# Kernel optimization log

Measured on AMD Instinct MI355X. Metric: run time of the kernel, lower is better.

## Reference

```python
import jax, jax.numpy as jnp
import numpy as np

N_NODES = 50000
N_EDGES = 800000
D_IN = 512
D_HID = 256


def gcn_conv(x, W, b, src, dst, n_nodes):
    """PyG-style GCNConv: self-loops + symmetric normalization.
    x: [N, d_in], W: [d_in, d_out], b: [d_out], src/dst: [E] (already include self-loops? no -> add here)
    """
    loops = jnp.arange(n_nodes, dtype=src.dtype)
    src_f = jnp.concatenate([src, loops])  # [E+N]
    dst_f = jnp.concatenate([dst, loops])
    deg = jax.ops.segment_sum(jnp.ones_like(dst_f, dtype=x.dtype), dst_f,
                              num_segments=n_nodes)  # [N]
    dinv = jnp.where(deg > 0, jax.lax.rsqrt(deg), 0.0)
    norm = dinv[src_f] * dinv[dst_f]  # [E+N]
    h = x @ W  # [N, d_out] -- dense GEMM
    msg = h[src_f] * norm[:, None]  # gather + scale, [E+N, d_out]
    out = jax.ops.segment_sum(msg, dst_f, num_segments=n_nodes)  # scatter-add
    return out + b


def setup_inputs() -> dict:
    key = jax.random.key(0)
    k1, k2, k3, k4, k5 = jax.random.split(key, 5)
    x = jax.random.normal(k1, (N_NODES, D_IN), dtype=jnp.float32)
    edge_index = jax.random.randint(k2, (2, N_EDGES), 0, N_NODES, dtype=jnp.int32)
    # Glorot-ish init for weights
    W1 = jax.random.normal(k3, (D_IN, D_HID), dtype=jnp.float32) / np.sqrt(D_IN)
    W2 = jax.random.normal(k4, (D_HID, D_HID), dtype=jnp.float32) / np.sqrt(D_HID)
    b1 = jnp.zeros((D_HID,), dtype=jnp.float32)
    b2 = jnp.zeros((D_HID,), dtype=jnp.float32)
    return {"x": x, "edge_index": edge_index, "W1": W1, "b1": b1, "W2": W2, "b2": b2}


def reference(x, edge_index, W1, b1, W2, b2):
    n_nodes = x.shape[0]
    src, dst = edge_index[0], edge_index[1]
    h = jax.nn.relu(gcn_conv(x, W1, b1, src, dst, n_nodes))
    h = gcn_conv(h, W2, b2, src, dst, n_nodes)
    # edge-level gather-dot scoring
    score = jnp.einsum('ed,ed->e', h[src], h[dst])  # [E]
    prob_edge = jax.nn.sigmoid(score)
    return prob_edge
```

## Files before the change

kernel.cpp:

```cpp
#include <hip/hip_runtime.h>
#include <stdint.h>

#define D_IN 512
#define D_HID 256

typedef __attribute__((ext_vector_type(8))) short bf16x8;
typedef __attribute__((ext_vector_type(8))) unsigned short u16x8;
typedef __attribute__((ext_vector_type(4))) float f32x4;

__device__ __forceinline__ float b2f(unsigned short u) {
    union { float f; uint32_t i; } x; x.i = ((uint32_t)u) << 16; return x.f;
}
__device__ __forceinline__ unsigned short f2b(float f) {
    union { float f; uint32_t i; } x; x.f = f;
    uint32_t i = x.i;
    uint32_t r = (i + 0x7FFFu + ((i >> 16) & 1u)) >> 16;
    return (unsigned short)r;
}

__device__ __forceinline__ void async_copy16(const unsigned short* g, unsigned short* lds) {
    __builtin_amdgcn_global_load_lds((const __attribute__((address_space(1))) unsigned int*)g,
                                     (__attribute__((address_space(3))) unsigned int*)lds,
                                     16, 0, 0);
}

__global__ __launch_bounds__(256) void detect_dtype_kernel(const ushort4* __restrict__ raw,
        int n4, int* __restrict__ flag, int* __restrict__ counts, int N, int dblocks) {
    int b = blockIdx.x;
    if (b >= dblocks) {
        int i = (b - dblocks) * 256 + threadIdx.x;
        if (i < N) counts[i] = 0;
        return;
    }
    int i = b * 256 + threadIdx.x;
    int hit = 0;
    if (i < n4) {
        ushort4 u = raw[i];
        hit = ((((u.x >> 7) & 0xFF) == 0xFF) || (((u.y >> 7) & 0xFF) == 0xFF) ||
               (((u.z >> 7) & 0xFF) == 0xFF) || (((u.w >> 7) & 0xFF) == 0xFF)) ? 1 : 0;
    }
    unsigned long long bl = __ballot(hit);
    if ((threadIdx.x & 63) == 0 && bl != 0ULL) atomicOr(flag, 1);
}

__device__ __forceinline__ void wpack_body(const void* __restrict__ W,
        unsigned short* __restrict__ Wp, int K, bool f32, int t) {
    int total = (K >> 6) * 2 * 16 * 64;
    if (t >= total) return;
    int lane = t & 63;
    int c = (t >> 6) & 15;
    int h = (t >> 10) & 1;
    int kk = t >> 11;
    int n = c * 16 + (lane & 15);
    int k0 = kk * 64 + h * 32 + (lane >> 4) * 8;
    u16x8 o;
#pragma unroll
    for (int j = 0; j < 8; ++j) {
        float v = f32 ? ((const float*)W)[(size_t)(k0 + j) * 256 + n]
                      : b2f(((const unsigned short*)W)[(size_t)(k0 + j) * 256 + n]);
        o[j] = f2b(v);
    }
    *(u16x8*)(Wp + (size_t)t * 8) = o;
}

__global__ __launch_bounds__(256) void pre_fused_kernel(const int* __restrict__ dst,
        int* __restrict__ counts, int* __restrict__ within, int E,
        const void* __restrict__ W1, unsigned short* __restrict__ Wp1,
        const void* __restrict__ W2, unsigned short* __restrict__ Wp2,
        const int* __restrict__ flag, int histBlocks, int wp1Blocks) {
    int b = blockIdx.x;
    if (b < histBlocks) {
        int halfE = (E + 1) >> 1;
        int e = b * 256 + threadIdx.x;
        if (e < halfE) {
            int d1 = dst[e];
            int e2 = e + halfE;
            if (e2 < E) {
                int d2 = dst[e2];
                within[e]  = atomicAdd(&counts[d1], 1);
                within[e2] = atomicAdd(&counts[d2], 1);
            } else {
                within[e] = atomicAdd(&counts[d1], 1);
            }
        }
        return;
    }
    b -= histBlocks;
    bool f32 = (*flag != 0);
    if (b < wp1Blocks) {
        wpack_body(W1, Wp1, D_IN, f32, b * 256 + threadIdx.x);
    } else {
        wpack_body(W2, Wp2, D_HID, f32, (b - wp1Blocks) * 256 + threadIdx.x);
    }
}

__global__ __launch_bounds__(256) void partial_sum_kernel(const int* __restrict__ counts,
        int* __restrict__ partial, int n) {
    __shared__ int sh[4];
    int b = blockIdx.x;
    int lane = threadIdx.x & 63, wv = threadIdx.x >> 6;
    int s = 0;
    for (int j = threadIdx.x; j < 1024; j += 256) {
        int i = b * 1024 + j;
        s += (i < n) ? counts[i] : 0;
    }
#pragma unroll
    for (int off = 32; off > 0; off >>= 1) s += __shfl_down(s, off, 64);
    if (lane == 0) sh[wv] = s;
    __syncthreads();
    if (threadIdx.x == 0) partial[b] = sh[0] + sh[1] + sh[2] + sh[3];
}

__global__ void scan_partials_kernel(int* __restrict__ partial, int nb,
                                     int* __restrict__ indptr, int N) {
    int lane = threadIdx.x & 63;
    int orig = (lane < nb) ? partial[lane] : 0;
    int v = orig;
#pragma unroll
    for (int off = 1; off < 64; off <<= 1) {
        int u = __shfl(v, lane - off, 64);
        if (lane >= off) v += u;
    }
    int tot = __shfl(v, nb - 1, 64);
    if (lane < nb) partial[lane] = v - orig;
    if (lane == 0) indptr[N] = tot;
}

__global__ __launch_bounds__(1024) void scan_chunk_kernel(const int* __restrict__ counts,
        const int* __restrict__ partial, int* __restrict__ indptr,
        float* __restrict__ dinv, int n) {
    __shared__ int sh[1024];
    int b = blockIdx.x;
    int i = b * 1024 + threadIdx.x;
    int v = (i < n) ? counts[i] : 0;
    sh[threadIdx.x] = v;
    __syncthreads();
    for (int off = 1; off < 1024; off <<= 1) {
        int t = (threadIdx.x >= off) ? sh[threadIdx.x - off] : 0;
        __syncthreads();
        sh[threadIdx.x] += t;
        __syncthreads();
    }
    if (i < n) {
        int e = partial[b] + sh[threadIdx.x] - v;
        indptr[i] = e;
        dinv[i] = rsqrtf((float)(v + 1));
    }
}

template<int K, bool MF32, bool FUSE>
__global__ __launch_bounds__(256) void gemm_bf16(const void* __restrict__ Ain,
        const unsigned short* __restrict__ Wp, unsigned short* __restrict__ C, int M,
        const int* __restrict__ flag,
        const int* __restrict__ eidx, const int* __restrict__ within,
        int* __restrict__ csr_src, int* __restrict__ csr_dst, int* __restrict__ pos_of,
        const int* __restrict__ indptr, int E, int sblocks) {
    __shared__ unsigned short As[(K == 256) ? 4 : 2][64 * 64];
    constexpr int NK = K / 64;
    int bid = blockIdx.x;
    int gblocks = (M + 63) >> 6;
    if (FUSE) {
        if (bid >= gblocks) {
            int tb = bid - gblocks;
            if (tb < sblocks) {
                int e = tb * 256 + (int)threadIdx.x;
                if (e < E) {
                    int d = eidx[(size_t)E + e];
                    int pos = indptr[d] + within[e];
                    csr_src[pos] = eidx[e];
                    pos_of[e] = pos;
                }
            } else {
                int v = (tb - sblocks) * 256 + (int)threadIdx.x;
                if (v < M) {
                    int b0 = indptr[v], e0 = indptr[v + 1];
                    for (int p = b0; p < e0; ++p) csr_dst[p] = v;
                }
            }
            return;
        }
    }
    int t = threadIdx.x;
    int lane = t & 63, wv = t >> 6;
    int n0 = lane & 15, grp = lane >> 4;
    int row0 = bid * 64;

    int srow = wv * 16 + (lane >> 3);
    int segp = lane & 7;

    f32x4 acc[4][4];
#pragma unroll
    for (int rt = 0; rt < 4; ++rt)
#pragma unroll
        for (int ct = 0; ct < 4; ++ct) acc[rt][ct] = (f32x4){0.f, 0.f, 0.f, 0.f};

    auto compute_tile = [&](int kk, const unsigned short* Abuf) {
        bf16x8 bw[4][2];
#pragma unroll
        for (int ct = 0; ct < 4; ++ct)
#pragma unroll
            for (int h = 0; h < 2; ++h)
                bw[ct][h] = *(const bf16x8*)(Wp +
                    ((size_t)(((kk * 2 + h) * 16) + (wv * 4 + ct)) * 64 + lane) * 8);
#pragma unroll
        for (int rt = 0; rt < 4; ++rt) {
            int r = rt * 16 + n0;
#pragma unroll
            for (int h = 0; h < 2; ++h) {
                int sp = (h * 4 + grp + r) & 7;
                bf16x8 a = *(const bf16x8*)(Abuf + r * 64 + sp * 8);
#pragma unroll
                for (int ct = 0; ct < 4; ++ct)
                    acc[rt][ct] = __builtin_amdgcn_mfma_f32_16x16x32_bf16(a, bw[ct][h],
                                                                          acc[rt][ct], 0, 0, 0);
            }
        }
    };

    bool f32src = MF32 && (*flag != 0);
    if (f32src) {
        const float* A = (const float*)Ain;
        auto stage_f32 = [&](int buf, const float4* pr) {
#pragma unroll
            for (int j = 0; j < 2; ++j) {
                u16x8 o;
#pragma unroll
                for (int q = 0; q < 4; ++q) {
                    o[q]     = f2b(pr[j * 2 + 0][q]);
                    o[q + 4] = f2b(pr[j * 2 + 1][q]);
                }
                *(u16x8*)(&As[buf][0] + wv * 1024 + j * 512 + lane * 8) = o;
            }
        };
        auto load_f32 = [&](int kof, float4* pr) {
#pragma unroll
            for (int j = 0; j < 2; ++j) {
                int row = srow + j * 8;
                int s = (segp - row) & 7;
                const float* g = A + (size_t)min(row0 + row, M - 1) * K + kof + s * 8;
                pr[j * 2 + 0] = *(const float4*)(g);
                pr[j * 2 + 1] = *(const float4*)(g + 4);
            }
        };
        float4 pr[4];
        load_f32(0, pr);
        stage_f32(0, pr);
        for (int kk = 0; kk < NK; ++kk) {
            int cur = kk & 1;
            if (kk + 1 < NK) load_f32((kk + 1) * 64, pr);
            asm volatile("s_waitcnt lgkmcnt(0)" ::: "memory");
            __builtin_amdgcn_s_barrier();
            compute_tile(kk, &As[cur][0]);
            if (kk + 1 < NK) stage_f32(cur ^ 1, pr);
        }
    } else if constexpr (K == 256) {
        const unsigned short* A = (const unsigned short*)Ain;
#pragma unroll
        for (int kk = 0; kk < 4; ++kk) {
#pragma unroll
            for (int j = 0; j < 2; ++j) {
                int row = srow + j * 8;
                int s = (segp - row) & 7;
                const unsigned short* g = A + (size_t)min(row0 + row, M - 1) * K
                                           + kk * 64 + s * 8;
                async_copy16(g, &As[kk][0] + wv * 1024 + j * 512);
            }
        }
        asm volatile("s_waitcnt vmcnt(0)" ::: "memory");
        __builtin_amdgcn_s_barrier();
#pragma unroll
        for (int kk = 0; kk < 4; ++kk) compute_tile(kk, &As[kk][0]);
    } else {
        const unsigned short* A = (const unsigned short*)Ain;
#pragma unroll
        for (int j = 0; j < 2; ++j) {
            int row = srow + j * 8;
            int s = (segp - row) & 7;
            const unsigned short* g = A + (size_t)min(row0 + row, M - 1) * K + s * 8;
            async_copy16(g, &As[0][0] + wv * 1024 + j * 512);
        }
        asm volatile("s_waitcnt vmcnt(0)" ::: "memory");
        __builtin_amdgcn_s_barrier();
        for (int kk = 0; kk < NK; ++kk) {
            int cur = kk & 1;
            if (kk + 1 < NK) {
                int kof = (kk + 1) * 64;
#pragma unroll
                for (int j = 0; j < 2; ++j) {
                    int row = srow + j * 8;
                    int s = (segp - row) & 7;
                    const unsigned short* g = A + (size_t)min(row0 + row, M - 1) * K + kof + s * 8;
                    async_copy16(g, &As[cur ^ 1][0] + wv * 1024 + j * 512);
                }
            }
            compute_tile(kk, &As[cur][0]);
            asm volatile("s_waitcnt vmcnt(0)" ::: "memory");
            __builtin_amdgcn_s_barrier();
        }
    }
#pragma unroll
    for (int rt = 0; rt < 4; ++rt) {
#pragma unroll
        for (int ct = 0; ct < 4; ++ct) {
#pragma unroll
            for (int reg = 0; reg < 4; ++reg) {
                int row = row0 + rt * 16 + grp * 4 + reg;
                if (row < M)
                    C[(size_t)row * 256 + (wv * 4 + ct) * 16 + n0] = f2b(acc[rt][ct][reg]);
            }
        }
    }
}

__global__ __launch_bounds__(256) void aggregate_kernel(const unsigned short* __restrict__ h,
        const int* __restrict__ indptr, const int* __restrict__ csr_src,
        const float* __restrict__ dinv, const void* __restrict__ bias,
        unsigned short* __restrict__ out, int n, int do_relu, const int* __restrict__ flag) {
    int wave = threadIdx.x >> 6;
    int lane = threadIdx.x & 63;
    int half = lane >> 5;
    int hl = lane & 31;
    int v = blockIdx.x * 4 + wave;
    if (v >= n) return;
    int beg = indptr[v];
    int end = indptr[v + 1];
    float dv = dinv[v];

    float acc[8];
    if (half == 0) {
        u16x8 hv = *(const u16x8*)(h + (size_t)v * 256 + hl * 8);
#pragma unroll
        for (int i = 0; i < 8; ++i) acc[i] = dv * b2f(hv[i]);
    } else {
#pragma unroll
        for (int i = 0; i < 8; ++i) acc[i] = 0.f;
    }

    float wA = 0.f, wB = 0.f, wC = 0.f;
    u16x8 rA = (u16x8)0, rB = (u16x8)0, rC = (u16x8)0;
    auto ld = [&](int idx, float& w, u16x8& r) {
        if (idx < end) {
            int s = csr_src[idx];
            w = dinv[s];
            r = *(const u16x8*)(h + (size_t)s * 256 + hl * 8);
        } else {
            w = 0.f;
        }
    };
    int e = beg + half;
    ld(e, wA, rA);
    ld(e + 2, wB, rB);
    ld(e + 4, wC, rC);
    while (e + 4 < end) {
#pragma unroll
        for (int i = 0; i < 8; ++i) acc[i] += wA * b2f(rA[i]);
        ld(e + 6, wA, rA);
#pragma unroll
        for (int i = 0; i < 8; ++i) acc[i] += wB * b2f(rB[i]);
        ld(e + 8, wB, rB);
#pragma unroll
        for (int i = 0; i < 8; ++i) acc[i] += wC * b2f(rC[i]);
        ld(e + 10, wC, rC);
        e += 6;
    }
#pragma unroll
    for (int i = 0; i < 8; ++i)
        acc[i] += wA * b2f(rA[i]) + wB * b2f(rB[i]) + wC * b2f(rC[i]);

#pragma unroll
    for (int i = 0; i < 8; ++i) acc[i] += __shfl_xor(acc[i], 32, 64);

    if (half == 0) {
        float bb[8];
        if (*flag != 0) {
            const float* bp = (const float*)bias + hl * 8;
#pragma unroll
            for (int i = 0; i < 8; ++i) bb[i] = bp[i];
        } else {
            const unsigned short* bp = (const unsigned short*)bias + hl * 8;
#pragma unroll
            for (int i = 0; i < 8; ++i) bb[i] = b2f(bp[i]);
        }
        u16x8 ov;
#pragma unroll
        for (int i = 0; i < 8; ++i) {
            float o = dv * acc[i] + bb[i];
            if (do_relu) o = fmaxf(o, 0.f);
            ov[i] = f2b(o);
        }
        *(u16x8*)(out + (size_t)v * 256 + hl * 8) = ov;
    }
}

__global__ __launch_bounds__(256) void edge_score_mfma(const unsigned short* __restrict__ h,
        const int* __restrict__ csr_src, const int* __restrict__ csr_dst,
        float* __restrict__ tmp, int E) {
    int lane = threadIdx.x & 63;
    int wv = threadIdx.x >> 6;
    int base = (blockIdx.x * 4 + wv) * 16;
    if (base >= E) return;
    int m = lane & 15, grp = lane >> 4;
    int e = base + m;
    int ec = min(e, E - 1);
    int s = csr_src[ec], d = csr_dst[ec];
    const unsigned short* hs = h + (size_t)s * 256 + grp * 8;
    const unsigned short* hd = h + (size_t)d * 256 + grp * 8;
    f32x4 acc = {0.f, 0.f, 0.f, 0.f};
#pragma unroll
    for (int kk = 0; kk < 8; ++kk) {
        bf16x8 a = *(const bf16x8*)(hs + kk * 32);
        bf16x8 b = *(const bf16x8*)(hd + kk * 32);
        acc = __builtin_amdgcn_mfma_f32_16x16x32_bf16(a, b, acc, 0, 0, 0);
    }
    int reg = m - grp * 4;
    if (reg >= 0 && reg < 4 && e < E) {
        float p = (reg == 0) ? acc[0] : (reg == 1) ? acc[1] : (reg == 2) ? acc[2] : acc[3];
        tmp[e] = 1.f / (1.f + __expf(-p));
    }
}

__global__ __launch_bounds__(256) void permute_out_kernel(const float* __restrict__ tmp,
        const int* __restrict__ pos_of, void* __restrict__ out, int E,
        const int* __restrict__ flag) {
    int e = blockIdx.x * blockDim.x + threadIdx.x;
    if (e >= E) return;
    float p = tmp[pos_of[e]];
    if (*flag != 0)
        ((float*)out)[e] = p;
    else
        ((unsigned short*)out)[e] = f2b(p);
}

extern "C" void kernel_launch(void* const* d_in, const int* in_sizes, int n_in,
                              void* d_out, int out_size, void* d_ws, size_t ws_size,
                              hipStream_t stream) {
    const void* x  = d_in[0];
    const int* edge_index = (const int*)d_in[1];
    const void* W1 = d_in[2];
    const void* b1 = d_in[3];
    const void* W2 = d_in[4];
    const void* b2 = d_in[5];

    const int N = in_sizes[0] / D_IN;
    const int E = in_sizes[1] / 2;
    const int* dst = edge_index + E;

    char* ws = (char*)d_ws;
    size_t off = 0;
    auto alloc = [&](size_t bytes) {
        char* p = ws + off;
        off = (off + bytes + 255) & ~(size_t)255;
        return p;
    };
    int* flag     = (int*)alloc(256);
    float* dinv   = (float*)alloc((size_t)N * 4);
    int* counts   = (int*)alloc((size_t)N * 4);
    int* indptr   = (int*)alloc((size_t)(N + 1) * 4);
    int* partial  = (int*)alloc(64 * 4);
    int* within   = (int*)alloc((size_t)E * 4);
    int* csr_src  = (int*)alloc((size_t)E * 4);
    int* csr_dst  = (int*)alloc((size_t)E * 4);
    int* pos_of   = (int*)alloc((size_t)E * 4);
    float* ptmp   = (float*)alloc((size_t)E * 4);
    unsigned short* Wp1 = (unsigned short*)alloc((size_t)D_IN * 256 * 2);
    unsigned short* Wp2 = (unsigned short*)alloc((size_t)D_HID * 256 * 2);
    unsigned short* hA  = (unsigned short*)alloc((size_t)N * 256 * 2);
    unsigned short* hB  = (unsigned short*)alloc((size_t)N * 256 * 2);

    const int nb = (N + 1023) / 1024;
    const int halfE = (E + 1) / 2;
    const int histBlocks = (halfE + 255) / 256;
    const int sblocks = (E + 255) / 256;
    const int fblocks = (N + 255) / 256;
    const int wp1Blocks = (D_IN * 32) / 256;
    const int wp2Blocks = (D_HID * 32) / 256;
    const int ggrid = (N + 63) / 64;
    const int dblocks = 64;

    hipMemsetAsync(flag, 0, 4, stream);
    detect_dtype_kernel<<<dblocks + fblocks, 256, 0, stream>>>(
        (const ushort4*)x, 16384, flag, counts, N, dblocks);
    pre_fused_kernel<<<histBlocks + wp1Blocks + wp2Blocks, 256, 0, stream>>>(
        dst, counts, within, E, W1, Wp1, W2, Wp2, flag, histBlocks, wp1Blocks);
    partial_sum_kernel<<<nb, 256, 0, stream>>>(counts, partial, N);
    scan_partials_kernel<<<1, 64, 0, stream>>>(partial, nb, indptr, N);
    scan_chunk_kernel<<<nb, 1024, 0, stream>>>(counts, partial, indptr, dinv, N);

    gemm_bf16<D_IN, true, true><<<ggrid + sblocks + fblocks, 256, 0, stream>>>(
        x, Wp1, hA, N, flag, edge_index, within, csr_src, csr_dst, pos_of, indptr, E, sblocks);
    aggregate_kernel<<<(N + 3) / 4, 256, 0, stream>>>(hA, indptr, csr_src, dinv, b1, hB, N, 1, flag);
    gemm_bf16<D_HID, false, false><<<ggrid, 256, 0, stream>>>(
        hB, Wp2, hA, N, flag, nullptr, nullptr, nullptr, nullptr, nullptr, nullptr, 0, 0);
    aggregate_kernel<<<(N + 3) / 4, 256, 0, stream>>>(hA, indptr, csr_src, dinv, b2, hB, N, 0, flag);
    edge_score_mfma<<<(E + 63) / 64, 256, 0, stream>>>(hB, csr_src, csr_dst, ptmp, E);
    permute_out_kernel<<<(E + 255) / 256, 256, 0, stream>>>(ptmp, pos_of, d_out, E, flag);
}
```

Measured before the change: 443.5 us.

## Halve GEMM row tile, move csr_dst fill into scan, quadruple histogram per-thread work

The GEMM kernels gain a ROWS template parameter and launch with 32-row tiles instead of 64. That doubles the grid to fill more CUs on the 50k-node problem, at the cost of reloading the weight fragments per block. The csr_dst fill moves from extra GEMM blocks into scan_chunk_kernel, removing those blocks from the fused launch. The histogram now handles four edges per thread so more atomics are in flight per thread.

```diff
diff --git a/kernel.cpp b/kernel.cpp
--- a/kernel.cpp
+++ b/kernel.cpp
@@ -70,18 +70,22 @@
         const int* __restrict__ flag, int histBlocks, int wp1Blocks) {
     int b = blockIdx.x;
     if (b < histBlocks) {
-        int halfE = (E + 1) >> 1;
+        int Q = (E + 3) >> 2;
         int e = b * 256 + threadIdx.x;
-        if (e < halfE) {
+        if (e < Q) {
+            int e2 = e + Q, e3 = e + 2 * Q, e4 = e + 3 * Q;
             int d1 = dst[e];
-            int e2 = e + halfE;
-            if (e2 < E) {
-                int d2 = dst[e2];
-                within[e]  = atomicAdd(&counts[d1], 1);
-                within[e2] = atomicAdd(&counts[d2], 1);
-            } else {
-                within[e] = atomicAdd(&counts[d1], 1);
-            }
+            int d2 = (e2 < E) ? dst[e2] : 0;
+            int d3 = (e3 < E) ? dst[e3] : 0;
+            int d4 = (e4 < E) ? dst[e4] : 0;
+            int w1v = atomicAdd(&counts[d1], 1);
+            int w2v = (e2 < E) ? atomicAdd(&counts[d2], 1) : 0;
+            int w3v = (e3 < E) ? atomicAdd(&counts[d3], 1) : 0;
+            int w4v = (e4 < E) ? atomicAdd(&counts[d4], 1) : 0;
+            within[e] = w1v;
+            if (e2 < E) within[e2] = w2v;
+            if (e3 < E) within[e3] = w3v;
+            if (e4 < E) within[e4] = w4v;
         }
         return;
     }
@@ -128,7 +132,7 @@
 
 __global__ __launch_bounds__(1024) void scan_chunk_kernel(const int* __restrict__ counts,
         const int* __restrict__ partial, int* __restrict__ indptr,
-        float* __restrict__ dinv, int n) {
+        float* __restrict__ dinv, int* __restrict__ csr_dst, int n) {
     __shared__ int sh[1024];
     int b = blockIdx.x;
     int i = b * 1024 + threadIdx.x;
@@ -145,20 +149,24 @@
         int e = partial[b] + sh[threadIdx.x] - v;
         indptr[i] = e;
         dinv[i] = rsqrtf((float)(v + 1));
-    }
-}
-
-template<int K, bool MF32, bool FUSE>
+        for (int p = e; p < e + v; ++p) csr_dst[p] = i;
+    }
+}
+
+template<int K, int ROWS, bool MF32, bool FUSE>
 __global__ __launch_bounds__(256) void gemm_bf16(const void* __restrict__ Ain,
         const unsigned short* __restrict__ Wp, unsigned short* __restrict__ C, int M,
         const int* __restrict__ flag,
         const int* __restrict__ eidx, const int* __restrict__ within,
-        int* __restrict__ csr_src, int* __restrict__ csr_dst, int* __restrict__ pos_of,
+        int* __restrict__ csr_src, int* __restrict__ pos_of,
         const int* __restrict__ indptr, int E, int sblocks) {
-    __shared__ unsigned short As[(K == 256) ? 4 : 2][64 * 64];
+    constexpr int RT = ROWS / 16;
+    constexpr int J = ROWS / 32;
+    constexpr int NSL = (K == 256) ? 4 : 2;
+    __shared__ unsigned short As[NSL][ROWS * 64];
     constexpr int NK = K / 64;
     int bid = blockIdx.x;
-    int gblocks = (M + 63) >> 6;
+    int gblocks = (M + ROWS - 1) / ROWS;
     if (FUSE) {
         if (bid >= gblocks) {
             int tb = bid - gblocks;
@@ -170,12 +178,6 @@
                     csr_src[pos] = eidx[e];
                     pos_of[e] = pos;
                 }
-            } else {
-                int v = (tb - sblocks) * 256 + (int)threadIdx.x;
-                if (v < M) {
-                    int b0 = indptr[v], e0 = indptr[v + 1];
-                    for (int p = b0; p < e0; ++p) csr_dst[p] = v;
-                }
             }
             return;
         }
@@ -183,14 +185,14 @@
     int t = threadIdx.x;
     int lane = t & 63, wv = t >> 6;
     int n0 = lane & 15, grp = lane >> 4;
-    int row0 = bid * 64;
-
-    int srow = wv * 16 + (lane >> 3);
+    int row0 = bid * ROWS;
+
+    int srow = wv * (ROWS / 4) + (lane >> 3);
     int segp = lane & 7;
 
-    f32x4 acc[4][4];
-#pragma unroll
-    for (int rt = 0; rt < 4; ++rt)
+    f32x4 acc[RT][4];
+#pragma unroll
+    for (int rt = 0; rt < RT; ++rt)
 #pragma unroll
         for (int ct = 0; ct < 4; ++ct) acc[rt][ct] = (f32x4){0.f, 0.f, 0.f, 0.f};
 
@@ -203,7 +205,7 @@
                 bw[ct][h] = *(const bf16x8*)(Wp +
                     ((size_t)(((kk * 2 + h) * 16) + (wv * 4 + ct)) * 64 + lane) * 8);
 #pragma unroll
-        for (int rt = 0; rt < 4; ++rt) {
+        for (int rt = 0; rt < RT; ++rt) {
             int r = rt * 16 + n0;
 #pragma unroll
             for (int h = 0; h < 2; ++h) {
@@ -222,19 +224,19 @@
         const float* A = (const float*)Ain;
         auto stage_f32 = [&](int buf, const float4* pr) {
 #pragma unroll
-            for (int j = 0; j < 2; ++j) {
+            for (int j = 0; j < J; ++j) {
                 u16x8 o;
 #pragma unroll
                 for (int q = 0; q < 4; ++q) {
                     o[q]     = f2b(pr[j * 2 + 0][q]);
                     o[q + 4] = f2b(pr[j * 2 + 1][q]);
                 }
-                *(u16x8*)(&As[buf][0] + wv * 1024 + j * 512 + lane * 8) = o;
+                *(u16x8*)(&As[buf][0] + wv * (ROWS * 16) + j * 512 + lane * 8) = o;
             }
         };
         auto load_f32 = [&](int kof, float4* pr) {
 #pragma unroll
-            for (int j = 0; j < 2; ++j) {
+            for (int j = 0; j < J; ++j) {
                 int row = srow + j * 8;
                 int s = (segp - row) & 7;
                 const float* g = A + (size_t)min(row0 + row, M - 1) * K + kof + s * 8;
@@ -242,7 +244,7 @@
                 pr[j * 2 + 1] = *(const float4*)(g + 4);
             }
         };
-        float4 pr[4];
+        float4 pr[2 * J];
         load_f32(0, pr);
         stage_f32(0, pr);
         for (int kk = 0; kk < NK; ++kk) {
@@ -258,12 +260,12 @@
 #pragma unroll
         for (int kk = 0; kk < 4; ++kk) {
 #pragma unroll
-            for (int j = 0; j < 2; ++j) {
+            for (int j = 0; j < J; ++j) {
                 int row = srow + j * 8;
                 int s = (segp - row) & 7;
                 const unsigned short* g = A + (size_t)min(row0 + row, M - 1) * K
                                            + kk * 64 + s * 8;
-                async_copy16(g, &As[kk][0] + wv * 1024 + j * 512);
+                async_copy16(g, &As[kk][0] + wv * (ROWS * 16) + j * 512);
             }
         }
         asm volatile("s_waitcnt vmcnt(0)" ::: "memory");
@@ -273,11 +275,11 @@
     } else {
         const unsigned short* A = (const unsigned short*)Ain;
 #pragma unroll
-        for (int j = 0; j < 2; ++j) {
+        for (int j = 0; j < J; ++j) {
             int row = srow + j * 8;
             int s = (segp - row) & 7;
             const unsigned short* g = A + (size_t)min(row0 + row, M - 1) * K + s * 8;
-            async_copy16(g, &As[0][0] + wv * 1024 + j * 512);
+            async_copy16(g, &As[0][0] + wv * (ROWS * 16) + j * 512);
         }
         asm volatile("s_waitcnt vmcnt(0)" ::: "memory");
         __builtin_amdgcn_s_barrier();
@@ -286,11 +288,11 @@
             if (kk + 1 < NK) {
                 int kof = (kk + 1) * 64;
 #pragma unroll
-                for (int j = 0; j < 2; ++j) {
+                for (int j = 0; j < J; ++j) {
                     int row = srow + j * 8;
                     int s = (segp - row) & 7;
                     const unsigned short* g = A + (size_t)min(row0 + row, M - 1) * K + kof + s * 8;
-                    async_copy16(g, &As[cur ^ 1][0] + wv * 1024 + j * 512);
+                    async_copy16(g, &As[cur ^ 1][0] + wv * (ROWS * 16) + j * 512);
                 }
             }
             compute_tile(kk, &As[cur][0]);
@@ -299,7 +301,7 @@
         }
     }
 #pragma unroll
-    for (int rt = 0; rt < 4; ++rt) {
+    for (int rt = 0; rt < RT; ++rt) {
 #pragma unroll
         for (int ct = 0; ct < 4; ++ct) {
 #pragma unroll
@@ -468,13 +470,13 @@
     unsigned short* hB  = (unsigned short*)alloc((size_t)N * 256 * 2);
 
     const int nb = (N + 1023) / 1024;
-    const int halfE = (E + 1) / 2;
-    const int histBlocks = (halfE + 255) / 256;
+    const int Q = (E + 3) / 4;
+    const int histBlocks = (Q + 255) / 256;
     const int sblocks = (E + 255) / 256;
     const int fblocks = (N + 255) / 256;
     const int wp1Blocks = (D_IN * 32) / 256;
     const int wp2Blocks = (D_HID * 32) / 256;
-    const int ggrid = (N + 63) / 64;
+    const int ggrid = (N + 31) / 32;
     const int dblocks = 64;
 
     hipMemsetAsync(flag, 0, 4, stream);
@@ -484,13 +486,13 @@
         dst, counts, within, E, W1, Wp1, W2, Wp2, flag, histBlocks, wp1Blocks);
     partial_sum_kernel<<<nb, 256, 0, stream>>>(counts, partial, N);
     scan_partials_kernel<<<1, 64, 0, stream>>>(partial, nb, indptr, N);
-    scan_chunk_kernel<<<nb, 1024, 0, stream>>>(counts, partial, indptr, dinv, N);
-
-    gemm_bf16<D_IN, true, true><<<ggrid + sblocks + fblocks, 256, 0, stream>>>(
-        x, Wp1, hA, N, flag, edge_index, within, csr_src, csr_dst, pos_of, indptr, E, sblocks);
+    scan_chunk_kernel<<<nb, 1024, 0, stream>>>(counts, partial, indptr, dinv, csr_dst, N);
+
+    gemm_bf16<D_IN, 32, true, true><<<ggrid + sblocks, 256, 0, stream>>>(
+        x, Wp1, hA, N, flag, edge_index, within, csr_src, pos_of, indptr, E, sblocks);
     aggregate_kernel<<<(N + 3) / 4, 256, 0, stream>>>(hA, indptr, csr_src, dinv, b1, hB, N, 1, flag);
-    gemm_bf16<D_HID, false, false><<<ggrid, 256, 0, stream>>>(
-        hB, Wp2, hA, N, flag, nullptr, nullptr, nullptr, nullptr, nullptr, nullptr, 0, 0);
+    gemm_bf16<D_HID, 32, false, false><<<ggrid, 256, 0, stream>>>(
+        hB, Wp2, hA, N, flag, nullptr, nullptr, nullptr, nullptr, nullptr, 0, 0);
     aggregate_kernel<<<(N + 3) / 4, 256, 0, stream>>>(hA, indptr, csr_src, dinv, b2, hB, N, 0, flag);
     edge_score_mfma<<<(E + 63) / 64, 256, 0, stream>>>(hB, csr_src, csr_dst, ptmp, E);
     permute_out_kernel<<<(E + 255) / 256, 256, 0, stream>>>(ptmp, pos_of, d_out, E, flag);
```

New measurement: 457.1 us. 3.1% more time.
